# Performance work log

Hardware: AMD Instinct MI355X
Metric: run time of the kernel (lower is better)

## Reference

```python
import jax, jax.numpy as jnp
import numpy as np

OUT_CHN, IN_CHN, K = 256, 256, 3
STRIDE, PADDING = 1, 1

def binary_activation(x):
    # STE: forward = sign(x), backward = piecewise-polynomial surrogate out3
    m1 = (x < -1).astype(x.dtype)
    m2 = (x < 0).astype(x.dtype)
    m3 = (x < 1).astype(x.dtype)
    out1 = -1.0 * m1 + (x * x + 2 * x) * (1 - m1)
    out2 = out1 * m2 + (-x * x + 2 * x) * (1 - m2)
    out3 = out2 * m3 + 1.0 * (1 - m3)
    return jax.lax.stop_gradient(jnp.sign(x)) - jax.lax.stop_gradient(out3) + out3

def setup_inputs() -> dict:
    key = jax.random.key(0)
    kx, kw = jax.random.split(key)
    x = jax.random.normal(kx, (32, IN_CHN, 56, 56), dtype=jnp.float32)
    # weights stored flat [N,1] as in the torch module, scaled by 0.001
    weights = jax.random.uniform(kw, (OUT_CHN * IN_CHN * K * K, 1), dtype=jnp.float32) * 0.001
    return {"x": x, "weights": weights}

def reference(x, weights):
    w = weights.reshape(OUT_CHN, IN_CHN, K, K)
    # STE for weights: forward = sign(w), backward = clamp(w,-1,1)
    clipped = jnp.clip(w, -1.0, 1.0)
    bw = jax.lax.stop_gradient(jnp.sign(w)) - jax.lax.stop_gradient(clipped) + clipped
    bx = binary_activation(x)
    y = jax.lax.conv_general_dilated(
        bx, bw,
        window_strides=(STRIDE, STRIDE),
        padding=[(PADDING, PADDING), (PADDING, PADDING)],
        dimension_numbers=("NCHW", "OIHW", "NCHW"),
    )
    return y
```

## Files before the change

### kernel.cpp

```cpp
#include <hip/hip_runtime.h>
#include <stdint.h>

#define N_BATCH 32
#define CHN     256
#define HW      56
#define HP      58
#define HPT     7

#define XPAD_CELLS (N_BATCH * HP * 2 * HP)
#define XPAD_U32   (XPAD_CELLS * 4)

__global__ __launch_bounds__(256) void binw_kernel(const float* __restrict__ wsrc,
                                                   uint32_t* __restrict__ wbits,
                                                   int* __restrict__ wpop) {
    __shared__ int part[9][4];
    int o = blockIdx.x;
    int t = threadIdx.x;
    int lane = t & 63, wv = t >> 6;
    const float* p = wsrc + ((size_t)o * 256 + t) * 9;
    float v[9];
#pragma unroll
    for (int tap = 0; tap < 9; tap++) v[tap] = p[tap];
#pragma unroll
    for (int tap = 0; tap < 9; tap++) {
        unsigned long long m = __ballot(v[tap] > 0.0f);
        if (lane == 0) {
            wbits[(size_t)(o * 9 + tap) * 8 + 2 * wv]     = (uint32_t)m;
            wbits[(size_t)(o * 9 + tap) * 8 + 2 * wv + 1] = (uint32_t)(m >> 32);
            part[tap][wv] = __builtin_popcountll(m);
        }
    }
    __syncthreads();
    if (t < 9) wpop[o * 9 + t] = part[t][0] + part[t][1] + part[t][2] + part[t][3];
}

__global__ __launch_bounds__(256) void binx_kernel(const float* __restrict__ x,
                                                   uint32_t* __restrict__ xpad) {
    int t    = threadIdx.x;
    int lane = t & 63;
    int fw   = blockIdx.x * 4 + (t >> 6);
    int k    = fw & 7;
    int q    = (fw >> 3) * 64 + lane;
    int n    = q / 784;
    int pq   = q - n * 784;

    const float4* src = (const float4*)x + ((size_t)(n * 256 + k * 32)) * 784 + pq;
    uint32_t b0 = 0, b1 = 0, b2 = 0, b3 = 0;
#pragma unroll
    for (int g = 0; g < 4; g++) {
        float4 v[8];
#pragma unroll
        for (int u = 0; u < 8; u++) v[u] = src[(size_t)(g * 8 + u) * 784];
#pragma unroll
        for (int u = 0; u < 8; u++) {
            int cc = g * 8 + u;
            b0 |= (v[u].x > 0.0f ? 1u : 0u) << cc;
            b1 |= (v[u].y > 0.0f ? 1u : 0u) << cc;
            b2 |= (v[u].z > 0.0f ? 1u : 0u) << cc;
            b3 |= (v[u].w > 0.0f ? 1u : 0u) << cc;
        }
    }
    int h  = pq / 14;
    int wq = pq - h * 14;
    int w0 = wq * 4;
    uint32_t cell = ((uint32_t)(n * HP + h + 1) * 2 + (k >> 2)) * HP + (w0 + 1);
    uint32_t* dst = xpad + (size_t)cell * 4 + (k & 3);
    dst[0] = b0; dst[4] = b1; dst[8] = b2; dst[12] = b3;
}

__global__ __launch_bounds__(256) void conv_kernel(const uint32_t* __restrict__ xpad,
                                                   const uint32_t* __restrict__ wbits,
                                                   const int* __restrict__ wpop,
                                                   float* __restrict__ out) {
    __shared__ uint4 sx[1044];

    int t    = threadIdx.x;
    int lane = t & 63;
    int wv   = t >> 6;
    int strip = blockIdx.x;
    int og    = blockIdx.y;
    int n     = blockIdx.z;
    int hb    = strip * HPT;
    int o     = __builtin_amdgcn_readfirstlane(og * 4 + wv);

    const uint4* xg = (const uint4*)xpad + (size_t)(n * HP + hb) * (2 * HP);
    for (int i = t; i < 1044; i += 256)
        sx[i] = xg[i];
    __syncthreads();

    int acc[HPT];
#pragma unroll
    for (int r = 0; r < HPT; r++) acc[r] = 0;

    const uint32_t* wa = wbits + (size_t)o * 72;
    const char* sxb = (const char*)sx + lane * 16;

#pragma unroll
    for (int h = 0; h < 2; h++) {
        uint32_t Wh[36];
#pragma unroll
        for (int tap = 0; tap < 9; tap++)
#pragma unroll
            for (int i = 0; i < 4; i++)
                Wh[tap * 4 + i] = wa[tap * 8 + h * 4 + i];
#pragma unroll
        for (int j = 0; j < HPT + 2; j++) {
            uint4 X0 = *(const uint4*)(sxb + ((j * 2 + h) * HP + 0) * 16);
            uint4 X1 = *(const uint4*)(sxb + ((j * 2 + h) * HP + 1) * 16);
            uint4 X2 = *(const uint4*)(sxb + ((j * 2 + h) * HP + 2) * 16);
#pragma unroll
            for (int dh = 0; dh < 3; dh++) {
                int r = j - dh;
                if (r >= 0 && r < HPT) {
#pragma unroll
                    for (int dw = 0; dw < 3; dw++) {
                        uint4 X = (dw == 0) ? X0 : (dw == 1) ? X1 : X2;
                        int ta = (dh * 3 + dw) * 4;
                        acc[r] += __builtin_popcount(X.x ^ Wh[ta + 0])
                                + __builtin_popcount(X.y ^ Wh[ta + 1])
                                + __builtin_popcount(X.z ^ Wh[ta + 2])
                                + __builtin_popcount(X.w ^ Wh[ta + 3]);
                    }
                }
            }
        }
    }

    if (lane < 56) {
        int w = lane;
        const int* wpa = wpop + (size_t)o * 9;
        int pa[9];
#pragma unroll
        for (int tp = 0; tp < 9; tp++) pa[tp] = wpa[tp];
        float* oa = out + (((size_t)n * 256 + o) * 56 + hb) * 56 + w;
        bool edge_w = (w == 0) | (w == 55);
#pragma unroll
        for (int r = 0; r < HPT; r++) {
            int hh = hb + r;
            int va = 2304 - 2 * acc[r];
            if (edge_w | (hh == 0) | (hh == 55)) {
                int ca = 0;
#pragma unroll
                for (int dh = -1; dh <= 1; dh++)
#pragma unroll
                    for (int dw = -1; dw <= 1; dw++)
                        if ((unsigned)(hh + dh) >= 56u || (unsigned)(w + dw) >= 56u)
                            ca += 256 - 2 * pa[(dh + 1) * 3 + (dw + 1)];
                va -= ca;
            }
            oa[(size_t)r * 56] = (float)va;
        }
    }
}

extern "C" void kernel_launch(void* const* d_in, const int* in_sizes, int n_in,
                              void* d_out, int out_size, void* d_ws, size_t ws_size,
                              hipStream_t stream) {
    const float* x    = (const float*)d_in[0];
    const float* wsrc = (const float*)d_in[1];
    float* out = (float*)d_out;

    uint32_t* xpad  = (uint32_t*)d_ws;
    uint32_t* wbits = xpad + XPAD_U32;
    int*      wpop  = (int*)(wbits + 256 * 9 * 8);

    hipMemsetAsync(xpad, 0, (size_t)XPAD_U32 * 4, stream);
    binw_kernel<<<256, 256, 0, stream>>>(wsrc, wbits, wpop);
    binx_kernel<<<784, 256, 0, stream>>>(x, xpad);
    conv_kernel<<<dim3(8, 64, N_BATCH), 256, 0, stream>>>(xpad, wbits, wpop, out);
}
```

Baseline: 368.9 us.

## Remap conv lanes to full 64-wide pixel tiles and split binarization over half-waves

The conv kernel now maps all 64 lanes to pixels spanning row-strip boundaries, so no lanes sit idle (before, 8 of 64 did). Each wave loops over 4 output channels, so one larger shared tile serves 16 channels per block, and the grid shrinks to 7x16x32. The binarize kernel splits each 32-channel group across two half-waves of 16 loads each, merged with a cross-lane shuffle, to raise memory parallelism. The trade-off is more LDS per block and a serial channel loop that reloads weights each iteration.

```diff
diff --git a/kernel.cpp b/kernel.cpp
--- a/kernel.cpp
+++ b/kernel.cpp
@@ -38,105 +38,127 @@
                                                    uint32_t* __restrict__ xpad) {
     int t    = threadIdx.x;
     int lane = t & 63;
-    int fw   = blockIdx.x * 4 + (t >> 6);
-    int k    = fw & 7;
-    int q    = (fw >> 3) * 64 + lane;
-    int n    = q / 784;
-    int pq   = q - n * 784;
+    int w    = blockIdx.x * 4 + (t >> 6);
+    int k    = w & 7;
+    int g32  = w >> 3;
+    int subq = lane & 31;
+    int hf   = lane >> 5;
+    int quad = g32 * 32 + subq;
+    int n    = quad / 784;
+    int pq   = quad - n * 784;
+    int c0   = k * 32 + hf * 16;
 
-    const float4* src = (const float4*)x + ((size_t)(n * 256 + k * 32)) * 784 + pq;
-    uint32_t b0 = 0, b1 = 0, b2 = 0, b3 = 0;
+    const float4* src = (const float4*)x + ((size_t)(n * 256 + c0)) * 784 + pq;
+    float4 v[16];
 #pragma unroll
-    for (int g = 0; g < 4; g++) {
-        float4 v[8];
+    for (int u = 0; u < 16; u++) v[u] = src[(size_t)u * 784];
+
+    uint32_t m0 = 0, m1 = 0, m2 = 0, m3 = 0;
 #pragma unroll
-        for (int u = 0; u < 8; u++) v[u] = src[(size_t)(g * 8 + u) * 784];
-#pragma unroll
-        for (int u = 0; u < 8; u++) {
-            int cc = g * 8 + u;
-            b0 |= (v[u].x > 0.0f ? 1u : 0u) << cc;
-            b1 |= (v[u].y > 0.0f ? 1u : 0u) << cc;
-            b2 |= (v[u].z > 0.0f ? 1u : 0u) << cc;
-            b3 |= (v[u].w > 0.0f ? 1u : 0u) << cc;
-        }
+    for (int u = 0; u < 16; u++) {
+        m0 |= (v[u].x > 0.0f ? 1u : 0u) << u;
+        m1 |= (v[u].y > 0.0f ? 1u : 0u) << u;
+        m2 |= (v[u].z > 0.0f ? 1u : 0u) << u;
+        m3 |= (v[u].w > 0.0f ? 1u : 0u) << u;
     }
-    int h  = pq / 14;
-    int wq = pq - h * 14;
-    int w0 = wq * 4;
-    uint32_t cell = ((uint32_t)(n * HP + h + 1) * 2 + (k >> 2)) * HP + (w0 + 1);
-    uint32_t* dst = xpad + (size_t)cell * 4 + (k & 3);
-    dst[0] = b0; dst[4] = b1; dst[8] = b2; dst[12] = b3;
+    uint32_t pA = m0 | (m1 << 16);
+    uint32_t pB = m2 | (m3 << 16);
+    uint32_t oA = __shfl_xor(pA, 32);
+    uint32_t oB = __shfl_xor(pB, 32);
+    if (hf == 0) {
+        uint32_t b0 = (pA & 0xffffu) | ((oA & 0xffffu) << 16);
+        uint32_t b1 = (pA >> 16)     | (oA & 0xffff0000u);
+        uint32_t b2 = (pB & 0xffffu) | ((oB & 0xffffu) << 16);
+        uint32_t b3 = (pB >> 16)     | (oB & 0xffff0000u);
+        int h  = pq / 14;
+        int wq = pq - h * 14;
+        int w0 = wq * 4;
+        uint32_t cell = ((uint32_t)(n * HP + h + 1) * 2 + (k >> 2)) * HP + (w0 + 1);
+        uint32_t* dst = xpad + (size_t)cell * 4 + (k & 3);
+        dst[0] = b0; dst[4] = b1; dst[8] = b2; dst[12] = b3;
+    }
 }
 
 __global__ __launch_bounds__(256) void conv_kernel(const uint32_t* __restrict__ xpad,
                                                    const uint32_t* __restrict__ wbits,
                                                    const int* __restrict__ wpop,
                                                    float* __restrict__ out) {
-    __shared__ uint4 sx[1044];
+    __shared__ uint4 sx[1856];
 
-    int t    = threadIdx.x;
-    int lane = t & 63;
-    int wv   = t >> 6;
+    int t     = threadIdx.x;
+    int lane  = t & 63;
+    int wv    = __builtin_amdgcn_readfirstlane(t >> 6);
     int strip = blockIdx.x;
     int og    = blockIdx.y;
     int n     = blockIdx.z;
-    int hb    = strip * HPT;
-    int o     = __builtin_amdgcn_readfirstlane(og * 4 + wv);
+    int ob    = og * 16 + wv * 4;
 
-    const uint4* xg = (const uint4*)xpad + (size_t)(n * HP + hb) * (2 * HP);
-    for (int i = t; i < 1044; i += 256)
-        sx[i] = xg[i];
+    const uint4* xg = (const uint4*)xpad + (size_t)(n * HP + strip * 7) * (2 * HP);
+    {
+        uint4 r[7];
+#pragma unroll
+        for (int i = 0; i < 7; i++) r[i] = xg[t + 256 * i];
+#pragma unroll
+        for (int i = 0; i < 7; i++) sx[t + 256 * i] = r[i];
+        if (t < 64) sx[1792 + t] = xg[1792 + t];
+    }
     __syncthreads();
 
-    int acc[HPT];
+    int b    = strip * 64 + lane;
+    int hb_i = b / 56;
+    int w    = b - hb_i * 56;
+    int r0   = (hb_i - strip) * 7;
+    const char* sxb = (const char*)sx + ((r0 * 2 * HP) + w) * 16;
+
+#pragma unroll 1
+    for (int oi = 0; oi < 4; oi++) {
+        int o = ob + oi;
+        const uint32_t* wa = wbits + (size_t)o * 72;
+
+        int acc[HPT];
 #pragma unroll
-    for (int r = 0; r < HPT; r++) acc[r] = 0;
-
-    const uint32_t* wa = wbits + (size_t)o * 72;
-    const char* sxb = (const char*)sx + lane * 16;
+        for (int r = 0; r < HPT; r++) acc[r] = 0;
 
 #pragma unroll
-    for (int h = 0; h < 2; h++) {
-        uint32_t Wh[36];
+        for (int h = 0; h < 2; h++) {
+            uint32_t Wh[36];
 #pragma unroll
-        for (int tap = 0; tap < 9; tap++)
+            for (int tap = 0; tap < 9; tap++)
 #pragma unroll
-            for (int i = 0; i < 4; i++)
-                Wh[tap * 4 + i] = wa[tap * 8 + h * 4 + i];
+                for (int i = 0; i < 4; i++)
+                    Wh[tap * 4 + i] = wa[tap * 8 + h * 4 + i];
 #pragma unroll
-        for (int j = 0; j < HPT + 2; j++) {
-            uint4 X0 = *(const uint4*)(sxb + ((j * 2 + h) * HP + 0) * 16);
-            uint4 X1 = *(const uint4*)(sxb + ((j * 2 + h) * HP + 1) * 16);
-            uint4 X2 = *(const uint4*)(sxb + ((j * 2 + h) * HP + 2) * 16);
+            for (int j = 0; j < HPT + 2; j++) {
+                uint4 X0 = *(const uint4*)(sxb + ((j * 2 + h) * HP + 0) * 16);
+                uint4 X1 = *(const uint4*)(sxb + ((j * 2 + h) * HP + 1) * 16);
+                uint4 X2 = *(const uint4*)(sxb + ((j * 2 + h) * HP + 2) * 16);
 #pragma unroll
-            for (int dh = 0; dh < 3; dh++) {
-                int r = j - dh;
-                if (r >= 0 && r < HPT) {
+                for (int dh = 0; dh < 3; dh++) {
+                    int r = j - dh;
+                    if (r >= 0 && r < HPT) {
 #pragma unroll
-                    for (int dw = 0; dw < 3; dw++) {
-                        uint4 X = (dw == 0) ? X0 : (dw == 1) ? X1 : X2;
-                        int ta = (dh * 3 + dw) * 4;
-                        acc[r] += __builtin_popcount(X.x ^ Wh[ta + 0])
-                                + __builtin_popcount(X.y ^ Wh[ta + 1])
-                                + __builtin_popcount(X.z ^ Wh[ta + 2])
-                                + __builtin_popcount(X.w ^ Wh[ta + 3]);
+                        for (int dw = 0; dw < 3; dw++) {
+                            uint4 X = (dw == 0) ? X0 : (dw == 1) ? X1 : X2;
+                            int ta = (dh * 3 + dw) * 4;
+                            acc[r] += __builtin_popcount(X.x ^ Wh[ta + 0])
+                                    + __builtin_popcount(X.y ^ Wh[ta + 1])
+                                    + __builtin_popcount(X.z ^ Wh[ta + 2])
+                                    + __builtin_popcount(X.w ^ Wh[ta + 3]);
+                        }
                     }
                 }
             }
         }
-    }
 
-    if (lane < 56) {
-        int w = lane;
         const int* wpa = wpop + (size_t)o * 9;
         int pa[9];
 #pragma unroll
         for (int tp = 0; tp < 9; tp++) pa[tp] = wpa[tp];
-        float* oa = out + (((size_t)n * 256 + o) * 56 + hb) * 56 + w;
+        float* oa = out + ((size_t)(n * 256 + o)) * 3136 + hb_i * 7 * 56 + w;
         bool edge_w = (w == 0) | (w == 55);
 #pragma unroll
         for (int r = 0; r < HPT; r++) {
-            int hh = hb + r;
+            int hh = hb_i * 7 + r;
             int va = 2304 - 2 * acc[r];
             if (edge_w | (hh == 0) | (hh == 55)) {
                 int ca = 0;
@@ -166,6 +188,6 @@
 
     hipMemsetAsync(xpad, 0, (size_t)XPAD_U32 * 4, stream);
     binw_kernel<<<256, 256, 0, stream>>>(wsrc, wbits, wpop);
-    binx_kernel<<<784, 256, 0, stream>>>(x, xpad);
-    conv_kernel<<<dim3(8, 64, N_BATCH), 256, 0, stream>>>(xpad, wbits, wpop, out);
+    binx_kernel<<<1568, 256, 0, stream>>>(x, xpad);
+    conv_kernel<<<dim3(7, 16, N_BATCH), 256, 0, stream>>>(xpad, wbits, wpop, out);
 }
```

Result: slower. 447.0 us (+21.2%).

## Process four output channels per wave to reuse the shared-memory input tile

Applied to the files above, without the earlier changes.

Each wave now loops over four output channels instead of one, so each block covers sixteen output channels and the grid's channel-group dimension shrinks from 64 to 16. The padded input strip is loaded into LDS once per block and reused by four times as many channels, cutting redundant global-to-LDS traffic and block launch overhead. Both channel halves are now processed in one pass, which holds all 72 weight words in registers and may increase register pressure. The grid has fewer blocks, which also lowers parallelism.

```diff
diff --git a/kernel.cpp b/kernel.cpp
--- a/kernel.cpp
+++ b/kernel.cpp
@@ -74,81 +74,88 @@
                                                    float* __restrict__ out) {
     __shared__ uint4 sx[1044];
 
-    int t    = threadIdx.x;
-    int lane = t & 63;
-    int wv   = t >> 6;
+    int t     = threadIdx.x;
+    int lane  = t & 63;
+    int wv    = t >> 6;
     int strip = blockIdx.x;
     int og    = blockIdx.y;
     int n     = blockIdx.z;
     int hb    = strip * HPT;
-    int o     = __builtin_amdgcn_readfirstlane(og * 4 + wv);
 
     const uint4* xg = (const uint4*)xpad + (size_t)(n * HP + hb) * (2 * HP);
     for (int i = t; i < 1044; i += 256)
         sx[i] = xg[i];
     __syncthreads();
 
-    int acc[HPT];
-#pragma unroll
-    for (int r = 0; r < HPT; r++) acc[r] = 0;
-
-    const uint32_t* wa = wbits + (size_t)o * 72;
     const char* sxb = (const char*)sx + lane * 16;
 
+#pragma unroll 1
+    for (int oi = 0; oi < 4; oi++) {
+        int o = __builtin_amdgcn_readfirstlane(og * 16 + wv * 4 + oi);
+        const uint32_t* wa = wbits + (size_t)o * 72;
+
+        uint32_t W[72];
 #pragma unroll
-    for (int h = 0; h < 2; h++) {
-        uint32_t Wh[36];
+        for (int i = 0; i < 72; i++) W[i] = wa[i];
+
+        int acc[HPT];
 #pragma unroll
-        for (int tap = 0; tap < 9; tap++)
-#pragma unroll
-            for (int i = 0; i < 4; i++)
-                Wh[tap * 4 + i] = wa[tap * 8 + h * 4 + i];
+        for (int r = 0; r < HPT; r++) acc[r] = 0;
+
 #pragma unroll
         for (int j = 0; j < HPT + 2; j++) {
-            uint4 X0 = *(const uint4*)(sxb + ((j * 2 + h) * HP + 0) * 16);
-            uint4 X1 = *(const uint4*)(sxb + ((j * 2 + h) * HP + 1) * 16);
-            uint4 X2 = *(const uint4*)(sxb + ((j * 2 + h) * HP + 2) * 16);
+            uint4 X0a = *(const uint4*)(sxb + ((j * 2 + 0) * HP + 0) * 16);
+            uint4 X1a = *(const uint4*)(sxb + ((j * 2 + 0) * HP + 1) * 16);
+            uint4 X2a = *(const uint4*)(sxb + ((j * 2 + 0) * HP + 2) * 16);
+            uint4 X0b = *(const uint4*)(sxb + ((j * 2 + 1) * HP + 0) * 16);
+            uint4 X1b = *(const uint4*)(sxb + ((j * 2 + 1) * HP + 1) * 16);
+            uint4 X2b = *(const uint4*)(sxb + ((j * 2 + 1) * HP + 2) * 16);
 #pragma unroll
             for (int dh = 0; dh < 3; dh++) {
                 int r = j - dh;
                 if (r >= 0 && r < HPT) {
 #pragma unroll
                     for (int dw = 0; dw < 3; dw++) {
-                        uint4 X = (dw == 0) ? X0 : (dw == 1) ? X1 : X2;
-                        int ta = (dh * 3 + dw) * 4;
-                        acc[r] += __builtin_popcount(X.x ^ Wh[ta + 0])
-                                + __builtin_popcount(X.y ^ Wh[ta + 1])
-                                + __builtin_popcount(X.z ^ Wh[ta + 2])
-                                + __builtin_popcount(X.w ^ Wh[ta + 3]);
+                        uint4 Xa = (dw == 0) ? X0a : (dw == 1) ? X1a : X2a;
+                        uint4 Xb = (dw == 0) ? X0b : (dw == 1) ? X1b : X2b;
+                        int ta = (dh * 3 + dw) * 8;
+                        acc[r] += __builtin_popcount(Xa.x ^ W[ta + 0])
+                                + __builtin_popcount(Xa.y ^ W[ta + 1])
+                                + __builtin_popcount(Xa.z ^ W[ta + 2])
+                                + __builtin_popcount(Xa.w ^ W[ta + 3])
+                                + __builtin_popcount(Xb.x ^ W[ta + 4])
+                                + __builtin_popcount(Xb.y ^ W[ta + 5])
+                                + __builtin_popcount(Xb.z ^ W[ta + 6])
+                                + __builtin_popcount(Xb.w ^ W[ta + 7]);
                     }
                 }
             }
         }
-    }
 
-    if (lane < 56) {
-        int w = lane;
-        const int* wpa = wpop + (size_t)o * 9;
-        int pa[9];
+        if (lane < 56) {
+            int w = lane;
+            const int* wpa = wpop + (size_t)o * 9;
+            int pa[9];
 #pragma unroll
-        for (int tp = 0; tp < 9; tp++) pa[tp] = wpa[tp];
-        float* oa = out + (((size_t)n * 256 + o) * 56 + hb) * 56 + w;
-        bool edge_w = (w == 0) | (w == 55);
+            for (int tp = 0; tp < 9; tp++) pa[tp] = wpa[tp];
+            float* oa = out + (((size_t)n * 256 + o) * 56 + hb) * 56 + w;
+            bool edge_w = (w == 0) | (w == 55);
 #pragma unroll
-        for (int r = 0; r < HPT; r++) {
-            int hh = hb + r;
-            int va = 2304 - 2 * acc[r];
-            if (edge_w | (hh == 0) | (hh == 55)) {
-                int ca = 0;
+            for (int r = 0; r < HPT; r++) {
+                int hh = hb + r;
+                int va = 2304 - 2 * acc[r];
+                if (edge_w | (hh == 0) | (hh == 55)) {
+                    int ca = 0;
 #pragma unroll
-                for (int dh = -1; dh <= 1; dh++)
+                    for (int dh = -1; dh <= 1; dh++)
 #pragma unroll
-                    for (int dw = -1; dw <= 1; dw++)
-                        if ((unsigned)(hh + dh) >= 56u || (unsigned)(w + dw) >= 56u)
-                            ca += 256 - 2 * pa[(dh + 1) * 3 + (dw + 1)];
-                va -= ca;
+                        for (int dw = -1; dw <= 1; dw++)
+                            if ((unsigned)(hh + dh) >= 56u || (unsigned)(w + dw) >= 56u)
+                                ca += 256 - 2 * pa[(dh + 1) * 3 + (dw + 1)];
+                    va -= ca;
+                }
+                oa[(size_t)r * 56] = (float)va;
             }
-            oa[(size_t)r * 56] = (float)va;
         }
     }
 }
@@ -167,5 +174,5 @@
     hipMemsetAsync(xpad, 0, (size_t)XPAD_U32 * 4, stream);
     binw_kernel<<<256, 256, 0, stream>>>(wsrc, wbits, wpop);
     binx_kernel<<<784, 256, 0, stream>>>(x, xpad);
-    conv_kernel<<<dim3(8, 64, N_BATCH), 256, 0, stream>>>(xpad, wbits, wpop, out);
+    conv_kernel<<<dim3(8, 16, N_BATCH), 256, 0, stream>>>(xpad, wbits, wpop, out);
 }
```

New measurement: 367.3 us. No clear change (-0.4%).
